# Kernel tuning notes

Measured on AMD Instinct MI355X. Metric: run time of the kernel, lower is better.

The kernel has to match this reference:

```python
import jax, jax.numpy as jnp
import numpy as np
from jax import lax


def _box_avg(x, k):
    # PyTorch F.avg_pool2d(kernel=k, stride=1, padding=k//2, count_include_pad=True):
    # sum over kxk window with zero padding, divided by k*k regardless of padding.
    p = k // 2
    s = lax.reduce_window(x, 0.0, lax.add,
                          window_dimensions=(1, 1, k, k),
                          window_strides=(1, 1, 1, 1),
                          padding=((0, 0), (0, 0), (p, p), (p, p)))
    return s / (k * k)


def setup_inputs() -> dict:
    key = jax.random.key(0)
    k1, k2 = jax.random.split(key)
    pred = jax.random.normal(k1, (16, 1, 1024, 1024), dtype=jnp.float32)
    mask = jax.random.uniform(k2, (16, 1, 1024, 1024), dtype=jnp.float32)
    return {"pred": pred, "mask": mask}


def reference(pred, mask):
    # multi-scale boundary weight
    w1 = jnp.abs(_box_avg(mask, 3) - mask)
    w2 = jnp.abs(_box_avg(mask, 15) - mask)
    w3 = jnp.abs(_box_avg(mask, 31) - mask)
    weit = 1.0 + 5.0 * (w1 + w2 + w3)

    # weighted BCE with logits (stable form, matches F.binary_cross_entropy_with_logits)
    bce = jnp.maximum(pred, 0.0) - pred * mask + jnp.log1p(jnp.exp(-jnp.abs(pred)))
    weit_sum = weit.sum(axis=(2, 3))  # [B, C]
    wbce = (weit * bce).sum(axis=(2, 3)) / weit_sum

    p = jax.nn.sigmoid(pred)
    inter = (p * mask * weit).sum(axis=(2, 3))
    union = ((p + mask) * weit).sum(axis=(2, 3))
    wiou = 1.0 - (inter + 1.0) / (union - inter + 1.0)

    # F.l1_loss(..., reduce=None) in torch defaults to mean reduction -> scalar
    mae = jnp.abs(p - mask).mean()
    wmae = (weit * mae).sum(axis=(2, 3)) / (weit - 1.0).sum(axis=(2, 3))

    return (0.7 * wbce + 0.7 * wiou + 0.7 * wmae).mean()
```

## Files before the change

kernel.cpp:

```cpp
#include <hip/hip_runtime.h>
#include <math.h>

#define BATCH 16
#define H 1024
#define W 1024
#define TILE 64
#define TILES_X (W / TILE)
#define TILES_Y (H / TILE)
#define NTILES  (TILES_X * TILES_Y)
#define HDIM 96
#define SCOLS 97
#define SEG  24


__device__ __forceinline__ float wave_sum_dpp(float x) {
    int t;
    t = __builtin_amdgcn_update_dpp(0, __float_as_int(x), 0x111, 0xf, 0xf, true);
    x += __int_as_float(t);
    t = __builtin_amdgcn_update_dpp(0, __float_as_int(x), 0x112, 0xf, 0xf, true);
    x += __int_as_float(t);
    t = __builtin_amdgcn_update_dpp(0, __float_as_int(x), 0x114, 0xf, 0xf, true);
    x += __int_as_float(t);
    t = __builtin_amdgcn_update_dpp(0, __float_as_int(x), 0x118, 0xf, 0xf, true);
    x += __int_as_float(t);
    t = __builtin_amdgcn_update_dpp(0, __float_as_int(x), 0x142, 0xf, 0xf, true);
    x += __int_as_float(t);
    t = __builtin_amdgcn_update_dpp(0, __float_as_int(x), 0x143, 0xf, 0xf, true);
    x += __int_as_float(t);
    return x;
}

__global__ __launch_bounds__(512, 6)
void adaptive_loss_main(const float* __restrict__ pred,
                        const float* __restrict__ mask,
                        float* __restrict__ part) {
    __shared__ float sat[HDIM * SCOLS];
    __shared__ float red[8][5];

    const int tid = threadIdx.x;
    const int b   = blockIdx.z;
    const int ty0 = blockIdx.y * TILE;
    const int tx0 = blockIdx.x * TILE;
    const float* mimg = mask + (size_t)b * H * W;
    const float* pimg = pred + (size_t)b * H * W;

    if (tid < 4 * HDIM) {
        const int row = tid >> 2, seg = tid & 3;
        const int gy  = ty0 - 16 + row;
        const int gx0 = tx0 - 16 + seg * SEG;
        const bool rowok = (gy >= 0) && (gy < H);
        const float* rp = mimg + (size_t)gy * W;

        float v[SEG];
        #pragma unroll
        for (int j = 0; j < 6; ++j) {
            int gx = gx0 + 4 * j;
            float4 t;
            if (rowok && gx >= 0 && gx < W) t = *(const float4*)(rp + gx);
            else                            t = make_float4(0.f, 0.f, 0.f, 0.f);
            v[4 * j + 0] = t.x; v[4 * j + 1] = t.y;
            v[4 * j + 2] = t.z; v[4 * j + 3] = t.w;
        }
        #pragma unroll
        for (int i = 1; i < SEG; ++i) v[i] += v[i - 1];
        float tot = v[SEG - 1];
        float inc = tot;
        float t1 = __shfl_up(inc, 1); if (seg >= 1) inc += t1;
        float t2 = __shfl_up(inc, 2); if (seg >= 2) inc += t2;
        const float off = inc - tot;
        const int base = row * SCOLS + seg * SEG;
        #pragma unroll
        for (int i = 0; i < SEG; ++i) sat[base + i] = v[i] + off;
    }
    __syncthreads();

    float4 m4[2], p4[2];
    #pragma unroll
    for (int i = 0; i < 2; ++i) {
        int y  = (tid >> 4) + 32 * i;
        int x4 = (tid & 15) << 2;
        size_t off = (size_t)(ty0 + y) * W + (tx0 + x4);
        m4[i] = *(const float4*)(mimg + off);
        p4[i] = *(const float4*)(pimg + off);
    }

    if (tid < 4 * HDIM) {
        const int col = tid >> 2, seg = tid & 3;
        const int base = (seg * SEG) * SCOLS + col;
        float v[SEG];
        #pragma unroll
        for (int i = 0; i < SEG; ++i) v[i] = sat[base + i * SCOLS];
        #pragma unroll
        for (int i = 1; i < SEG; ++i) v[i] += v[i - 1];
        float tot = v[SEG - 1];
        float inc = tot;
        float t1 = __shfl_up(inc, 1); if (seg >= 1) inc += t1;
        float t2 = __shfl_up(inc, 2); if (seg >= 2) inc += t2;
        const float off = inc - tot;
        #pragma unroll
        for (int i = 0; i < SEG; ++i) sat[base + i * SCOLS] = v[i] + off;
    }
    __syncthreads();

    float s_w = 0.0f, s_wb = 0.0f, s_in = 0.0f, s_un = 0.0f, s_mae = 0.0f;

    __builtin_amdgcn_s_setprio(1);
    #pragma unroll
    for (int i = 0; i < 2; ++i) {
        const int rc  = (tid >> 4) + 32 * i + 16;
        const int x0c = ((tid & 15) << 2) + 16;

        float w[4] = {0.f, 0.f, 0.f, 0.f};

        #pragma unroll
        for (int j = 0; j < 3; ++j) {
            constexpr int PP[3] = {1, 7, 15};
            constexpr float INV[3] = {1.0f / 9.0f, 1.0f / 225.0f, 1.0f / 961.0f};
            const int p = PP[j];
            const int bt = (rc + p) * SCOLS + x0c - 16;
            const int bb = (rc - p - 1) * SCOLS + x0c - 16;
            #pragma unroll
            for (int q = 0; q < 4; ++q) {
                float s = sat[bt + (16 + p + q)] - sat[bb + (16 + p + q)]
                        - sat[bt + (15 - p + q)] + sat[bb + (15 - p + q)];
                w[q] += fabsf(s * INV[j] - (&m4[i].x)[q]);
            }
        }

        #pragma unroll
        for (int q = 0; q < 4; ++q) {
            float m  = (&m4[i].x)[q];
            float pr = (&p4[i].x)[q];
            float weit = 1.0f + 5.0f * w[q];
            float t    = __expf(-fabsf(pr));
            float bce  = fmaxf(pr, 0.0f) - pr * m + __logf(1.0f + t);
            float u    = __builtin_amdgcn_rcpf(1.0f + t);
            float sig  = (pr >= 0.0f) ? u : 1.0f - u;

            s_w   += weit;
            s_wb  += weit * bce;
            s_in  += sig * m * weit;
            s_un  += (sig + m) * weit;
            s_mae += fabsf(sig - m);
        }
    }
    __builtin_amdgcn_s_setprio(0);

    s_w   = wave_sum_dpp(s_w);
    s_wb  = wave_sum_dpp(s_wb);
    s_in  = wave_sum_dpp(s_in);
    s_un  = wave_sum_dpp(s_un);
    s_mae = wave_sum_dpp(s_mae);

    int wave = tid >> 6, lane = tid & 63;
    if (lane == 63) {
        red[wave][0] = s_w;  red[wave][1] = s_wb; red[wave][2] = s_in;
        red[wave][3] = s_un; red[wave][4] = s_mae;
    }
    __syncthreads();
    if (tid < 5) {
        float r = 0.0f;
        #pragma unroll
        for (int wv = 0; wv < 8; ++wv) r += red[wv][tid];
        const int tile = blockIdx.y * TILES_X + blockIdx.x;
        part[((size_t)tid * BATCH + b) * NTILES + tile] = r;
    }
}

__global__ __launch_bounds__(1024)
void adaptive_loss_finalize(const float* __restrict__ part,
                            float* __restrict__ out) {
    __shared__ float sums[BATCH][5];
    const int wv   = threadIdx.x >> 6;
    const int lane = threadIdx.x & 63;

    float v[5];
    #pragma unroll
    for (int c = 0; c < 5; ++c) {
        float s = 0.0f;
        #pragma unroll
        for (int r = 0; r < NTILES / 64; ++r)
            s += part[((size_t)c * BATCH + wv) * NTILES + r * 64 + lane];
        v[c] = s;
    }
    #pragma unroll
    for (int off = 32; off > 0; off >>= 1) {
        #pragma unroll
        for (int c = 0; c < 5; ++c) v[c] += __shfl_down(v[c], off);
    }
    if (lane == 0) {
        #pragma unroll
        for (int c = 0; c < 5; ++c) sums[wv][c] = v[c];
    }
    __syncthreads();

    if (threadIdx.x == 0) {
        float smae = 0.0f;
        for (int b = 0; b < BATCH; ++b) smae += sums[b][4];
        float mae = smae / (float)((size_t)BATCH * H * W);
        float tot = 0.0f;
        for (int b = 0; b < BATCH; ++b) {
            float Sw  = sums[b][0];
            float Swb = sums[b][1];
            float Si  = sums[b][2];
            float Su  = sums[b][3];
            float wbce = Swb / Sw;
            float wiou = 1.0f - (Si + 1.0f) / (Su - Si + 1.0f);
            float wmae = mae * Sw / (Sw - (float)(H * W));
            tot += 0.7f * (wbce + wiou + wmae);
        }
        out[0] = tot / (float)BATCH;
    }
}

extern "C" void kernel_launch(void* const* d_in, const int* in_sizes, int n_in,
                              void* d_out, int out_size, void* d_ws, size_t ws_size,
                              hipStream_t stream) {
    const float* pred = (const float*)d_in[0];
    const float* mask = (const float*)d_in[1];
    float* part = (float*)d_ws;

    dim3 grid(TILES_X, TILES_Y, BATCH);
    adaptive_loss_main<<<grid, 512, 0, stream>>>(pred, mask, part);
    adaptive_loss_finalize<<<1, 1024, 0, stream>>>(part, (float*)d_out);
}
```

Before: 164.9 us.

## Process two vertical tiles per block with prefetch of second tile's loads

Each block now handles two vertically stacked 64x64 tiles. While the first tile's column scan and loss computation run, it issues the global loads for the second tile's halo rows and pixel data, hiding memory latency behind compute. The grid is halved and the finalize kernel is adjusted to the new partial count. In exchange, register pressure rises from holding prefetched data under the 512x6 launch bound, the halo between adjacent tiles is still reloaded rather than reused, and the extra barriers serialise the two tiles.

```diff
diff --git a/kernel.cpp b/kernel.cpp
--- a/kernel.cpp
+++ b/kernel.cpp
@@ -6,8 +6,9 @@
 #define W 1024
 #define TILE 64
 #define TILES_X (W / TILE)
-#define TILES_Y (H / TILE)
-#define NTILES  (TILES_X * TILES_Y)
+#define TPB 2
+#define TYG (H / TILE / TPB)
+#define NTG (TILES_X * TYG)
 #define HDIM 96
 #define SCOLS 97
 #define SEG  24
@@ -30,80 +31,60 @@
     return x;
 }
 
-__global__ __launch_bounds__(512, 6)
-void adaptive_loss_main(const float* __restrict__ pred,
-                        const float* __restrict__ mask,
-                        float* __restrict__ part) {
-    __shared__ float sat[HDIM * SCOLS];
-    __shared__ float red[8][5];
-
-    const int tid = threadIdx.x;
-    const int b   = blockIdx.z;
-    const int ty0 = blockIdx.y * TILE;
-    const int tx0 = blockIdx.x * TILE;
-    const float* mimg = mask + (size_t)b * H * W;
-    const float* pimg = pred + (size_t)b * H * W;
-
-    if (tid < 4 * HDIM) {
-        const int row = tid >> 2, seg = tid & 3;
-        const int gy  = ty0 - 16 + row;
-        const int gx0 = tx0 - 16 + seg * SEG;
-        const bool rowok = (gy >= 0) && (gy < H);
-        const float* rp = mimg + (size_t)gy * W;
-
-        float v[SEG];
-        #pragma unroll
-        for (int j = 0; j < 6; ++j) {
-            int gx = gx0 + 4 * j;
-            float4 t;
-            if (rowok && gx >= 0 && gx < W) t = *(const float4*)(rp + gx);
-            else                            t = make_float4(0.f, 0.f, 0.f, 0.f);
-            v[4 * j + 0] = t.x; v[4 * j + 1] = t.y;
-            v[4 * j + 2] = t.z; v[4 * j + 3] = t.w;
-        }
-        #pragma unroll
-        for (int i = 1; i < SEG; ++i) v[i] += v[i - 1];
-        float tot = v[SEG - 1];
-        float inc = tot;
-        float t1 = __shfl_up(inc, 1); if (seg >= 1) inc += t1;
-        float t2 = __shfl_up(inc, 2); if (seg >= 2) inc += t2;
-        const float off = inc - tot;
-        const int base = row * SCOLS + seg * SEG;
-        #pragma unroll
-        for (int i = 0; i < SEG; ++i) sat[base + i] = v[i] + off;
-    }
-    __syncthreads();
-
-    float4 m4[2], p4[2];
-    #pragma unroll
-    for (int i = 0; i < 2; ++i) {
-        int y  = (tid >> 4) + 32 * i;
-        int x4 = (tid & 15) << 2;
-        size_t off = (size_t)(ty0 + y) * W + (tx0 + x4);
-        m4[i] = *(const float4*)(mimg + off);
-        p4[i] = *(const float4*)(pimg + off);
-    }
-
-    if (tid < 4 * HDIM) {
-        const int col = tid >> 2, seg = tid & 3;
-        const int base = (seg * SEG) * SCOLS + col;
-        float v[SEG];
-        #pragma unroll
-        for (int i = 0; i < SEG; ++i) v[i] = sat[base + i * SCOLS];
-        #pragma unroll
-        for (int i = 1; i < SEG; ++i) v[i] += v[i - 1];
-        float tot = v[SEG - 1];
-        float inc = tot;
-        float t1 = __shfl_up(inc, 1); if (seg >= 1) inc += t1;
-        float t2 = __shfl_up(inc, 2); if (seg >= 2) inc += t2;
-        const float off = inc - tot;
-        #pragma unroll
-        for (int i = 0; i < SEG; ++i) sat[base + i * SCOLS] = v[i] + off;
-    }
-    __syncthreads();
-
-    float s_w = 0.0f, s_wb = 0.0f, s_in = 0.0f, s_un = 0.0f, s_mae = 0.0f;
-
+__device__ __forceinline__ void load_scan_row(const float* __restrict__ mimg,
+                                              int ty0, int tx0, int row, int seg,
+                                              float v[SEG]) {
+    const int gy  = ty0 - 16 + row;
+    const int gx0 = tx0 - 16 + seg * SEG;
+    const bool rowok = (gy >= 0) && (gy < H);
+    const float* rp = mimg + (size_t)gy * W;
+    #pragma unroll
+    for (int j = 0; j < 6; ++j) {
+        int gx = gx0 + 4 * j;
+        float4 t;
+        if (rowok && gx >= 0 && gx < W) t = *(const float4*)(rp + gx);
+        else                            t = make_float4(0.f, 0.f, 0.f, 0.f);
+        v[4 * j + 0] = t.x; v[4 * j + 1] = t.y;
+        v[4 * j + 2] = t.z; v[4 * j + 3] = t.w;
+    }
+}
+
+__device__ __forceinline__ void scan_and_store_row(float v[SEG], int row, int seg,
+                                                   float* __restrict__ sat) {
+    #pragma unroll
+    for (int i = 1; i < SEG; ++i) v[i] += v[i - 1];
+    float tot = v[SEG - 1];
+    float inc = tot;
+    float t1 = __shfl_up(inc, 1); if (seg >= 1) inc += t1;
+    float t2 = __shfl_up(inc, 2); if (seg >= 2) inc += t2;
+    const float off = inc - tot;
+    const int base = row * SCOLS + seg * SEG;
+    #pragma unroll
+    for (int i = 0; i < SEG; ++i) sat[base + i] = v[i] + off;
+}
+
+__device__ __forceinline__ void col_scan(float* __restrict__ sat, int tid) {
+    const int col = tid >> 2, seg = tid & 3;
+    const int base = (seg * SEG) * SCOLS + col;
+    float v[SEG];
+    #pragma unroll
+    for (int i = 0; i < SEG; ++i) v[i] = sat[base + i * SCOLS];
+    #pragma unroll
+    for (int i = 1; i < SEG; ++i) v[i] += v[i - 1];
+    float tot = v[SEG - 1];
+    float inc = tot;
+    float t1 = __shfl_up(inc, 1); if (seg >= 1) inc += t1;
+    float t2 = __shfl_up(inc, 2); if (seg >= 2) inc += t2;
+    const float off = inc - tot;
+    #pragma unroll
+    for (int i = 0; i < SEG; ++i) sat[base + i * SCOLS] = v[i] + off;
+}
+
+__device__ __forceinline__ void compute_tile(const float* __restrict__ sat,
+                                             const float4 m4[2], const float4 p4[2],
+                                             int tid,
+                                             float& s_w, float& s_wb, float& s_in,
+                                             float& s_un, float& s_mae) {
     __builtin_amdgcn_s_setprio(1);
     #pragma unroll
     for (int i = 0; i < 2; ++i) {
@@ -145,6 +126,68 @@
         }
     }
     __builtin_amdgcn_s_setprio(0);
+}
+
+__global__ __launch_bounds__(512, 6)
+void adaptive_loss_main(const float* __restrict__ pred,
+                        const float* __restrict__ mask,
+                        float* __restrict__ part) {
+    __shared__ float sat[HDIM * SCOLS];
+    __shared__ float red[8][5];
+
+    const int tid = threadIdx.x;
+    const int b   = blockIdx.z;
+    const int ty0a = (blockIdx.y * TPB) * TILE;
+    const int ty0b = ty0a + TILE;
+    const int tx0  = blockIdx.x * TILE;
+    const float* mimg = mask + (size_t)b * H * W;
+    const float* pimg = pred + (size_t)b * H * W;
+
+    const int srow = tid >> 2, sseg = tid & 3;
+
+    float s_w = 0.0f, s_wb = 0.0f, s_in = 0.0f, s_un = 0.0f, s_mae = 0.0f;
+
+    if (tid < 4 * HDIM) {
+        float va[SEG];
+        load_scan_row(mimg, ty0a, tx0, srow, sseg, va);
+        scan_and_store_row(va, srow, sseg, sat);
+    }
+    __syncthreads();
+
+    float4 m4a[2], p4a[2];
+    #pragma unroll
+    for (int i = 0; i < 2; ++i) {
+        int y  = (tid >> 4) + 32 * i;
+        int x4 = (tid & 15) << 2;
+        size_t off = (size_t)(ty0a + y) * W + (tx0 + x4);
+        m4a[i] = *(const float4*)(mimg + off);
+        p4a[i] = *(const float4*)(pimg + off);
+    }
+    float vb[SEG];
+    if (tid < 4 * HDIM) load_scan_row(mimg, ty0b, tx0, srow, sseg, vb);
+    float4 m4b[2], p4b[2];
+    #pragma unroll
+    for (int i = 0; i < 2; ++i) {
+        int y  = (tid >> 4) + 32 * i;
+        int x4 = (tid & 15) << 2;
+        size_t off = (size_t)(ty0b + y) * W + (tx0 + x4);
+        m4b[i] = *(const float4*)(mimg + off);
+        p4b[i] = *(const float4*)(pimg + off);
+    }
+
+    if (tid < 4 * HDIM) col_scan(sat, tid);
+    __syncthreads();
+
+    compute_tile(sat, m4a, p4a, tid, s_w, s_wb, s_in, s_un, s_mae);
+    __syncthreads();
+
+    if (tid < 4 * HDIM) scan_and_store_row(vb, srow, sseg, sat);
+    __syncthreads();
+
+    if (tid < 4 * HDIM) col_scan(sat, tid);
+    __syncthreads();
+
+    compute_tile(sat, m4b, p4b, tid, s_w, s_wb, s_in, s_un, s_mae);
 
     s_w   = wave_sum_dpp(s_w);
     s_wb  = wave_sum_dpp(s_wb);
@@ -162,8 +205,8 @@
         float r = 0.0f;
         #pragma unroll
         for (int wv = 0; wv < 8; ++wv) r += red[wv][tid];
-        const int tile = blockIdx.y * TILES_X + blockIdx.x;
-        part[((size_t)tid * BATCH + b) * NTILES + tile] = r;
+        const int group = blockIdx.y * TILES_X + blockIdx.x;
+        part[((size_t)tid * BATCH + b) * NTG + group] = r;
     }
 }
 
@@ -179,8 +222,8 @@
     for (int c = 0; c < 5; ++c) {
         float s = 0.0f;
         #pragma unroll
-        for (int r = 0; r < NTILES / 64; ++r)
-            s += part[((size_t)c * BATCH + wv) * NTILES + r * 64 + lane];
+        for (int r = 0; r < NTG / 64; ++r)
+            s += part[((size_t)c * BATCH + wv) * NTG + r * 64 + lane];
         v[c] = s;
     }
     #pragma unroll
@@ -220,7 +263,7 @@
     const float* mask = (const float*)d_in[1];
     float* part = (float*)d_ws;
 
-    dim3 grid(TILES_X, TILES_Y, BATCH);
+    dim3 grid(TILES_X, TYG, BATCH);
     adaptive_loss_main<<<grid, 512, 0, stream>>>(pred, mask, part);
     adaptive_loss_finalize<<<1, 1024, 0, stream>>>(part, (float*)d_out);
 }
```

Measured after the change: 295.6 us. 1.79x slower.
